# Optimization experiments

Measured on AMD Instinct MI355X. Metric: run time of the kernel, lower is better.

Reference implementation:

```python
import jax, jax.numpy as jnp
import numpy as np

B, N, D = 4, 2048, 1024
H = 16
HD = D // H


def setup_inputs() -> dict:
    key = jax.random.key(0)
    ks = jax.random.split(key, 6)
    x = jax.random.normal(ks[0], (B, N, D), dtype=jnp.float32)
    # additive causal mask: 0 on/below diagonal, -inf above
    neg = jnp.float32(-1e9)
    causal_mask = jnp.where(jnp.triu(jnp.ones((N, N), dtype=bool), k=1), neg, 0.0).astype(jnp.float32)
    s = 1.0 / np.sqrt(D)
    Wqkv = jax.random.normal(ks[1], (D, 3 * D), dtype=jnp.float32) * s
    bqkv = jax.random.normal(ks[2], (3 * D,), dtype=jnp.float32) * 0.01
    Wproj = jax.random.normal(ks[3], (D, D), dtype=jnp.float32) * s
    bproj = jax.random.normal(ks[4], (D,), dtype=jnp.float32) * 0.01
    return {"x": x, "causal_mask": causal_mask, "Wqkv": Wqkv, "bqkv": bqkv, "Wproj": Wproj, "bproj": bproj}


def reference(x, causal_mask, Wqkv, bqkv, Wproj, bproj):
    b, n, d = x.shape
    qkv = x @ Wqkv + bqkv  # [B,N,3D]
    qkv = qkv.reshape(b, n, 3, H, HD).transpose(2, 0, 3, 1, 4)  # [3,B,H,N,HD]
    q, k, v = qkv[0], qkv[1], qkv[2]
    scale = HD ** -0.5
    attn = jnp.einsum('bhqd,bhkd->bhqk', q, k) * scale  # [B,H,N,N]
    attn = attn + causal_mask  # broadcast [N,N] -> [B,H,N,N]
    attn = jax.nn.softmax(attn, axis=-1)
    out = jnp.einsum('bhqk,bhkd->bhqd', attn, v)  # [B,H,N,HD]
    out = out.transpose(0, 2, 1, 3).reshape(b, n, d)
    return out @ Wproj + bproj
```

## Files before the change

kernel.cpp:

```cpp
#include <hip/hip_runtime.h>
#include <hip/hip_bf16.h>

typedef unsigned short u16;
typedef unsigned int u32;
typedef __attribute__((ext_vector_type(8))) short bf16x8;
typedef __attribute__((ext_vector_type(4))) float f32x4;
typedef __attribute__((ext_vector_type(16))) float f32x16;

#define AS1(p) ((const __attribute__((address_space(1))) void*)(p))
#define AS3(p) ((__attribute__((address_space(3))) void*)(p))
#define STG(src, dst) __builtin_amdgcn_global_load_lds(AS1(src), AS3(dst), 16, 0, 0)

#if __has_builtin(__builtin_amdgcn_exp2f)
#define EXP2F(x) __builtin_amdgcn_exp2f(x)
#else
#define EXP2F(x) exp2f(x)
#endif

static __device__ __forceinline__ float b2f(u16 u) {
  union { unsigned int i; float f; } v; v.i = ((unsigned int)u) << 16; return v.f;
}
static __device__ __forceinline__ u16 f2b(float f) {
  union { float f; unsigned int i; } v; v.f = f;
  unsigned int r = v.i + 0x7FFFu + ((v.i >> 16) & 1u);
  return (u16)(r >> 16);
}
static __device__ __forceinline__ u32 cvt_pk_bf16(float lo, float hi) {
  u32 r;
  asm("v_cvt_pk_bf16_f32 %0, %1, %2" : "=v"(r) : "v"(lo), "v"(hi));
  return r;
}
static __device__ __forceinline__ void permswap(u32& a, u32& b) {
  asm("v_permlane32_swap_b32 %0, %1" : "+v"(a), "+v"(b));
}

__global__ __launch_bounds__(256) void cast_f32_bf16(const float* __restrict__ src,
                                                     u16* __restrict__ dst, int n8) {
  int stride = gridDim.x * blockDim.x;
  for (int i = blockIdx.x * blockDim.x + threadIdx.x; i < n8; i += stride) {
    const float4* s = (const float4*)(src + (size_t)i * 8);
    float4 a = s[0], b = s[1];
    bf16x8 o;
    o[0] = (short)f2b(a.x); o[1] = (short)f2b(a.y); o[2] = (short)f2b(a.z); o[3] = (short)f2b(a.w);
    o[4] = (short)f2b(b.x); o[5] = (short)f2b(b.y); o[6] = (short)f2b(b.z); o[7] = (short)f2b(b.w);
    *(bf16x8*)(dst + (size_t)i * 8) = o;
  }
}

__global__ __launch_bounds__(256) void transpose_w(const float* __restrict__ src,
                                                   u16* __restrict__ dst,
                                                   int R, int C) {
  __shared__ float tile[32][33];
  int c0 = blockIdx.x * 32, r0 = blockIdx.y * 32;
  int tx = threadIdx.x, ty = threadIdx.y;
  for (int i = ty; i < 32; i += 8) tile[i][tx] = src[(size_t)(r0 + i) * C + c0 + tx];
  __syncthreads();
  for (int i = ty; i < 32; i += 8) dst[(size_t)(c0 + i) * R + r0 + tx] = f2b(tile[tx][i]);
}

__global__ __launch_bounds__(256) void transpose_v(const u16* __restrict__ qkv,
                                                   u16* __restrict__ VT) {
  const int N = 2048, TD = 3072, D = 1024;
  int bh = blockIdx.y, n0 = blockIdx.x * 64;
  int b = bh >> 4, h = bh & 15;
  int tid = threadIdx.x;
  __shared__ u16 tl[64][72];
  #pragma unroll
  for (int i = 0; i < 16; ++i) {
    int idx = tid + i * 256;
    int nl = idx >> 6, dd = idx & 63;
    tl[dd][nl] = qkv[(size_t)(b * N + n0 + nl) * TD + 2 * D + h * 64 + dd];
  }
  __syncthreads();
  #pragma unroll
  for (int i = 0; i < 16; ++i) {
    int idx = tid + i * 256;
    int dd = idx >> 6, nl = idx & 63;
    VT[((size_t)bh * 64 + dd) * N + n0 + nl] = tl[dd][nl];
  }
}

template <typename OutT>
__global__ __launch_bounds__(256) void gemm_bt_bias(
    const u16* __restrict__ A,
    const u16* __restrict__ BT,
    const float* __restrict__ bias,
    OutT* __restrict__ C,
    int M, int N, int K) {
  __shared__ alignas(16) u16 Als[128 * 32];
  __shared__ alignas(16) u16 Bls[128 * 32];
  const int m0 = blockIdx.x * 128, n0 = blockIdx.y * 128;
  const int t = threadIdx.x;
  const int w = t >> 6, lane = t & 63;
  const int wr = w >> 1, wc = w & 1;
  const int rlo = lane & 15, g = lane >> 4;

  f32x4 acc[4][4] = {};

  const int r0 = t >> 2;
  const int c0 = (t & 3) << 3;
  const u16* aSrc = A + (size_t)(m0 + r0) * K + c0;
  const u16* bSrc = BT + (size_t)(n0 + r0) * K + c0;

  for (int k0 = 0; k0 < K; k0 += 32) {
    __builtin_amdgcn_global_load_lds(AS1(aSrc + k0), AS3(&Als[t * 8]), 16, 0, 0);
    __builtin_amdgcn_global_load_lds(AS1(aSrc + (size_t)64 * K + k0), AS3(&Als[(t + 256) * 8]), 16, 0, 0);
    __builtin_amdgcn_global_load_lds(AS1(bSrc + k0), AS3(&Bls[t * 8]), 16, 0, 0);
    __builtin_amdgcn_global_load_lds(AS1(bSrc + (size_t)64 * K + k0), AS3(&Bls[(t + 256) * 8]), 16, 0, 0);
    __syncthreads();

    bf16x8 a[4], b[4];
    #pragma unroll
    for (int m = 0; m < 4; ++m)
      a[m] = *(const bf16x8*)&Als[(wr * 64 + m * 16 + rlo) * 32 + g * 8];
    #pragma unroll
    for (int n = 0; n < 4; ++n)
      b[n] = *(const bf16x8*)&Bls[(wc * 64 + n * 16 + rlo) * 32 + g * 8];
    #pragma unroll
    for (int m = 0; m < 4; ++m)
      #pragma unroll
      for (int n = 0; n < 4; ++n)
        acc[m][n] = __builtin_amdgcn_mfma_f32_16x16x32_bf16(a[m], b[n], acc[m][n], 0, 0, 0);
    __syncthreads();
  }

  #pragma unroll
  for (int n = 0; n < 4; ++n) {
    const int col = n0 + wc * 64 + n * 16 + rlo;
    const float bv = bias[col];
    #pragma unroll
    for (int m = 0; m < 4; ++m) {
      const int row = m0 + wr * 64 + m * 16 + g * 4;
      #pragma unroll
      for (int i = 0; i < 4; ++i) {
        float r = acc[m][n][i] + bv;
        if constexpr (sizeof(OutT) == 2)
          C[(size_t)(row + i) * N + col] = (OutT)f2b(r);
        else
          C[(size_t)(row + i) * N + col] = (OutT)r;
      }
    }
  }
}

__global__ __launch_bounds__(256, 2) void attn_fwd(
    const u16* __restrict__ qkv,
    const u16* __restrict__ VT,
    u16* __restrict__ O) {
  const int N = 2048, TD = 3072, D = 1024;
  const int bid = blockIdx.x;
  const int qp = bid >> 6, bh = bid & 63;
  const int b = bh >> 4, h = bh & 15;
  const int t = threadIdx.x, w = t >> 6, lane = t & 63;
  const int l31 = lane & 31, hi = lane >> 5;
  const int qh = w >> 1, st = w & 1;

  __shared__ alignas(16) u16 pool16[2][2][64 * 64];
  __shared__ float rsLds[2][32];
  float* poolf = (float*)&pool16[0][0][0];

  const int c1 = t, c2 = t + 256;
  const int r1 = c1 >> 3, sc1 = ((c1 & 7) ^ (r1 & 7)) * 8;
  const int r2 = c2 >> 3, sc2 = ((c2 & 7) ^ (r2 & 7)) * 8;
  const u16* kbase = qkv + (size_t)(b * N) * TD + D + h * 64;
  const u16* vbase = VT + (size_t)bh * 64 * N;

#define ASTAGE(buf, j0) do { \
    STG(kbase + (size_t)((j0) + r1) * TD + sc1, &pool16[buf][0][c1 * 8]); \
    STG(kbase + (size_t)((j0) + r2) * TD + sc2, &pool16[buf][0][c2 * 8]); \
    STG(vbase + (size_t)r1 * N + (j0) + sc1, &pool16[buf][1][c1 * 8]); \
    STG(vbase + (size_t)r2 * N + (j0) + sc2, &pool16[buf][1][c2 * 8]); } while (0)

  const float L2E = 1.44269504089f;
  const float NSH = -23.0830992f;

  for (int pass = 0; pass < 2; ++pass) {
    const int qt = pass ? (15 - qp) : qp;
    const int qbw = qt * 128 + qh * 64;

    bf16x8 qf[2][4];
    #pragma unroll
    for (int qs = 0; qs < 2; ++qs) {
      const u16* qp_ = qkv + ((size_t)(b * N) + qbw + qs * 32 + l31) * TD + h * 64 + hi * 8;
      #pragma unroll
      for (int c = 0; c < 4; ++c) {
        bf16x8 v = *(const bf16x8*)(qp_ + c * 16);
        #pragma unroll
        for (int j = 0; j < 8; ++j)
          v[j] = (short)f2b(b2f((u16)v[j]) * 0.125f);
        qf[qs][c] = v;
      }
    }

    f32x16 o_acc[2][2] = {};
    float psum[2] = {0.f, 0.f};
    const int jend = qt * 128 + 64;

    ASTAGE(0, 0);
    __syncthreads();

    int cur = 0;
    for (int j0 = 0; j0 <= jend; j0 += 64) {
      if (j0 + 64 <= jend) ASTAGE(cur ^ 1, j0 + 64);

      const int sb2 = j0 + st * 32;
      if (sb2 <= qbw + 63) {
        bf16x8 kf[4];
        {
          const int row = st * 32 + l31, sw = (row & 7) << 3;
          #pragma unroll
          for (int c = 0; c < 4; ++c)
            kf[c] = *(const bf16x8*)&pool16[cur][0][row * 64 + ((c * 16 + hi * 8) ^ sw)];
        }
        bf16x8 vf[2][2];
        #pragma unroll
        for (int dt = 0; dt < 2; ++dt) {
          const int row = dt * 32 + l31, sw = (row & 7) << 3;
          #pragma unroll
          for (int kc = 0; kc < 2; ++kc)
            vf[kc][dt] = *(const bf16x8*)&pool16[cur][1][row * 64 + ((st * 32 + kc * 16 + hi * 8) ^ sw)];
        }

        #pragma unroll
        for (int qs = 0; qs < 2; ++qs) {
          if (qs == 0 && sb2 > qbw + 31) continue;
          const int qr = qbw + qs * 32 + l31;
          f32x16 S = {};
          __builtin_amdgcn_s_setprio(1);
          #pragma unroll
          for (int c = 0; c < 4; ++c)
            S = __builtin_amdgcn_mfma_f32_32x32x16_bf16(kf[c], qf[qs][c], S, 0, 0, 0);
          __builtin_amdgcn_s_setprio(0);
          if (sb2 + 31 > qbw + qs * 32) {
            const int kvb = sb2 + 4 * hi;
            #pragma unroll
            for (int r = 0; r < 16; ++r)
              if (kvb + (r & 3) + 8 * (r >> 2) > qr) S[r] = -1e30f;
          }
          float p[16];
          #pragma unroll
          for (int r = 0; r < 16; ++r) p[r] = EXP2F(fmaf(S[r], L2E, NSH));
          float ps = 0.f;
          #pragma unroll
          for (int r = 0; r < 16; ++r) ps += p[r];
          psum[qs] += ps;
          u32 wq[8];
          #pragma unroll
          for (int i = 0; i < 8; ++i) wq[i] = cvt_pk_bf16(p[2 * i], p[2 * i + 1]);
          permswap(wq[0], wq[2]); permswap(wq[1], wq[3]);
          permswap(wq[4], wq[6]); permswap(wq[5], wq[7]);
          union { u32 u[4]; bf16x8 v; } pa0, pa1;
          pa0.u[0] = wq[0]; pa0.u[1] = wq[1]; pa0.u[2] = wq[2]; pa0.u[3] = wq[3];
          pa1.u[0] = wq[4]; pa1.u[1] = wq[5]; pa1.u[2] = wq[6]; pa1.u[3] = wq[7];
          __builtin_amdgcn_s_setprio(1);
          #pragma unroll
          for (int dt = 0; dt < 2; ++dt) {
            o_acc[qs][dt] = __builtin_amdgcn_mfma_f32_32x32x16_bf16(pa0.v, vf[0][dt], o_acc[qs][dt], 0, 0, 0);
            o_acc[qs][dt] = __builtin_amdgcn_mfma_f32_32x32x16_bf16(pa1.v, vf[1][dt], o_acc[qs][dt], 0, 0, 0);
          }
          __builtin_amdgcn_s_setprio(0);
        }
      }
      __syncthreads();
      cur ^= 1;
    }

    float rsown[2];
    #pragma unroll
    for (int qs = 0; qs < 2; ++qs)
      rsown[qs] = psum[qs] + __shfl_xor(psum[qs], 32, 64);

    #pragma unroll
    for (int qs = 0; qs < 2; ++qs) {
      if (st != qs) {
        #pragma unroll
        for (int dt = 0; dt < 2; ++dt)
          #pragma unroll
          for (int r = 0; r < 16; ++r)
            poolf[qh * 2048 + (dt * 16 + r) * 64 + lane] = o_acc[qs][dt][r];
        rsLds[qh][l31] = rsown[qs];
      }
      __syncthreads();
      if (st == qs) {
        const float inv = 1.0f / (rsown[qs] + rsLds[qh][l31]);
        #pragma unroll
        for (int r = 0; r < 16; ++r) {
          const int qrow = (r & 3) + 8 * (r >> 2) + 4 * hi;
          const float invq = __shfl(inv, qrow, 64);
          const int q = qbw + qs * 32 + qrow;
          #pragma unroll
          for (int dt = 0; dt < 2; ++dt) {
            const float val = o_acc[qs][dt][r] + poolf[qh * 2048 + (dt * 16 + r) * 64 + lane];
            O[((size_t)(b * N) + q) * D + h * 64 + dt * 32 + l31] = f2b(val * invq);
          }
        }
      }
      __syncthreads();
    }
  }
#undef ASTAGE
}

extern "C" void kernel_launch(void* const* d_in, const int* in_sizes, int n_in,
                              void* d_out, int out_size, void* d_ws, size_t ws_size,
                              hipStream_t stream) {
  const float* x     = (const float*)d_in[0];
  const float* Wqkv  = (const float*)d_in[2];
  const float* bqkv  = (const float*)d_in[3];
  const float* Wproj = (const float*)d_in[4];
  const float* bproj = (const float*)d_in[5];
  float* out = (float*)d_out;

  const int B = 4, N = 2048, D = 1024, H = 16;
  const int BN = B * N;
  const int TD = 3 * D;

  char* ws = (char*)d_ws;
  u16* qkv    = (u16*)(ws);
  u16* vt     = (u16*)(ws + 50331648);
  u16* aout   = (u16*)(ws + 67108864);
  u16* wqkvT  = (u16*)(ws + 83886080);
  u16* wprojT = (u16*)(ws + 90177536);
  u16* xb     = (u16*)(ws + 92274688);

  cast_f32_bf16<<<2048, 256, 0, stream>>>(x, xb, BN * D / 8);
  transpose_w<<<dim3(TD / 32, D / 32), dim3(32, 8), 0, stream>>>(Wqkv, wqkvT, D, TD);
  transpose_w<<<dim3(D / 32, D / 32), dim3(32, 8), 0, stream>>>(Wproj, wprojT, D, D);
  gemm_bt_bias<u16><<<dim3(BN / 128, TD / 128), 256, 0, stream>>>(xb, wqkvT, bqkv, qkv, BN, TD, D);
  transpose_v<<<dim3(N / 64, B * H), 256, 0, stream>>>(qkv, vt);
  attn_fwd<<<512, 256, 0, stream>>>(qkv, vt, aout);
  gemm_bt_bias<float><<<dim3(BN / 128, D / 128), 256, 0, stream>>>(aout, wprojT, bproj, out, BN, D, D);
}
```

Measured before the change: 185.9 us.

## Merge prep kernels and write transposed V from QKV GEMM epilogue

Folds the x cast and both weight transposes into one launch that picks its role from the block index. The separate V-transpose kernel is removed: the QKV GEMM epilogue now also writes V columns straight into the transposed VT layout, using 8-byte stores of four consecutive rows. This saves two launches and a full read and write pass over V. In exchange the GEMM epilogue takes on extra scattered stores.

After: 178.6 us. 3.9% less time.

```diff
diff --git a/kernel.cpp b/kernel.cpp
--- a/kernel.cpp
+++ b/kernel.cpp
@@ -34,59 +34,41 @@
   asm("v_permlane32_swap_b32 %0, %1" : "+v"(a), "+v"(b));
 }
 
-__global__ __launch_bounds__(256) void cast_f32_bf16(const float* __restrict__ src,
-                                                     u16* __restrict__ dst, int n8) {
-  int stride = gridDim.x * blockDim.x;
-  for (int i = blockIdx.x * blockDim.x + threadIdx.x; i < n8; i += stride) {
-    const float4* s = (const float4*)(src + (size_t)i * 8);
-    float4 a = s[0], b = s[1];
-    bf16x8 o;
-    o[0] = (short)f2b(a.x); o[1] = (short)f2b(a.y); o[2] = (short)f2b(a.z); o[3] = (short)f2b(a.w);
-    o[4] = (short)f2b(b.x); o[5] = (short)f2b(b.y); o[6] = (short)f2b(b.z); o[7] = (short)f2b(b.w);
-    *(bf16x8*)(dst + (size_t)i * 8) = o;
+__global__ __launch_bounds__(256) void prep(const float* __restrict__ x, u16* __restrict__ xb,
+                                            const float* __restrict__ Wqkv, u16* __restrict__ wqkvT,
+                                            const float* __restrict__ Wproj, u16* __restrict__ wprojT) {
+  __shared__ float tile[32][33];
+  const int bid = blockIdx.x, t = threadIdx.x;
+  if (bid < 2048) {
+    const int n8 = 8192 * 1024 / 8;
+    for (int i = bid * 256 + t; i < n8; i += 2048 * 256) {
+      const float4* s = (const float4*)(x + (size_t)i * 8);
+      float4 a = s[0], b = s[1];
+      bf16x8 o;
+      o[0] = (short)f2b(a.x); o[1] = (short)f2b(a.y); o[2] = (short)f2b(a.z); o[3] = (short)f2b(a.w);
+      o[4] = (short)f2b(b.x); o[5] = (short)f2b(b.y); o[6] = (short)f2b(b.z); o[7] = (short)f2b(b.w);
+      *(bf16x8*)(xb + (size_t)i * 8) = o;
+    }
+  } else {
+    const float* src; u16* dst; int R, C, cx, ry;
+    if (bid < 5120) { const int l = bid - 2048; src = Wqkv; dst = wqkvT; R = 1024; C = 3072; cx = l % 96; ry = l / 96; }
+    else            { const int l = bid - 5120; src = Wproj; dst = wprojT; R = 1024; C = 1024; cx = l & 31; ry = l >> 5; }
+    const int c0 = cx * 32, r0 = ry * 32;
+    const int tx = t & 31, ty = t >> 5;
+    for (int i = ty; i < 32; i += 8) tile[i][tx] = src[(size_t)(r0 + i) * C + c0 + tx];
+    __syncthreads();
+    for (int i = ty; i < 32; i += 8) dst[(size_t)(c0 + i) * R + r0 + tx] = f2b(tile[tx][i]);
   }
 }
 
-__global__ __launch_bounds__(256) void transpose_w(const float* __restrict__ src,
-                                                   u16* __restrict__ dst,
-                                                   int R, int C) {
-  __shared__ float tile[32][33];
-  int c0 = blockIdx.x * 32, r0 = blockIdx.y * 32;
-  int tx = threadIdx.x, ty = threadIdx.y;
-  for (int i = ty; i < 32; i += 8) tile[i][tx] = src[(size_t)(r0 + i) * C + c0 + tx];
-  __syncthreads();
-  for (int i = ty; i < 32; i += 8) dst[(size_t)(c0 + i) * R + r0 + tx] = f2b(tile[tx][i]);
-}
-
-__global__ __launch_bounds__(256) void transpose_v(const u16* __restrict__ qkv,
-                                                   u16* __restrict__ VT) {
-  const int N = 2048, TD = 3072, D = 1024;
-  int bh = blockIdx.y, n0 = blockIdx.x * 64;
-  int b = bh >> 4, h = bh & 15;
-  int tid = threadIdx.x;
-  __shared__ u16 tl[64][72];
-  #pragma unroll
-  for (int i = 0; i < 16; ++i) {
-    int idx = tid + i * 256;
-    int nl = idx >> 6, dd = idx & 63;
-    tl[dd][nl] = qkv[(size_t)(b * N + n0 + nl) * TD + 2 * D + h * 64 + dd];
-  }
-  __syncthreads();
-  #pragma unroll
-  for (int i = 0; i < 16; ++i) {
-    int idx = tid + i * 256;
-    int dd = idx >> 6, nl = idx & 63;
-    VT[((size_t)bh * 64 + dd) * N + n0 + nl] = tl[dd][nl];
-  }
-}
-
-template <typename OutT>
+template <typename OutT, bool WVT>
 __global__ __launch_bounds__(256) void gemm_bt_bias(
     const u16* __restrict__ A,
     const u16* __restrict__ BT,
     const float* __restrict__ bias,
     OutT* __restrict__ C,
-    int M, int N, int K) {
+    int M, int N, int K,
+    u16* __restrict__ vt) {
   __shared__ alignas(16) u16 Als[128 * 32];
   __shared__ alignas(16) u16 Bls[128 * 32];
   const int m0 = blockIdx.x * 128, n0 = blockIdx.y * 128;
@@ -131,13 +113,28 @@
     #pragma unroll
     for (int m = 0; m < 4; ++m) {
       const int row = m0 + wr * 64 + m * 16 + g * 4;
+      u16 tmp[4];
       #pragma unroll
       for (int i = 0; i < 4; ++i) {
         float r = acc[m][n][i] + bv;
-        if constexpr (sizeof(OutT) == 2)
-          C[(size_t)(row + i) * N + col] = (OutT)f2b(r);
-        else
+        if constexpr (sizeof(OutT) == 2) {
+          const u16 hv = f2b(r);
+          C[(size_t)(row + i) * N + col] = (OutT)hv;
+          if constexpr (WVT) tmp[i] = hv;
+        } else {
           C[(size_t)(row + i) * N + col] = (OutT)r;
+        }
+      }
+      if constexpr (WVT) {
+        if (col >= 2048) {
+          const int cv = col - 2048;
+          const int h = cv >> 6, dd = cv & 63;
+          const int b = row >> 11, nloc = row & 2047;
+          uint2 pv;
+          pv.x = (u32)tmp[0] | ((u32)tmp[1] << 16);
+          pv.y = (u32)tmp[2] | ((u32)tmp[3] << 16);
+          *(uint2*)&vt[(((size_t)(b * 16 + h)) * 64 + dd) * 2048 + nloc] = pv;
+        }
       }
     }
   }
@@ -323,11 +320,8 @@
   u16* wprojT = (u16*)(ws + 90177536);
   u16* xb     = (u16*)(ws + 92274688);
 
-  cast_f32_bf16<<<2048, 256, 0, stream>>>(x, xb, BN * D / 8);
-  transpose_w<<<dim3(TD / 32, D / 32), dim3(32, 8), 0, stream>>>(Wqkv, wqkvT, D, TD);
-  transpose_w<<<dim3(D / 32, D / 32), dim3(32, 8), 0, stream>>>(Wproj, wprojT, D, D);
-  gemm_bt_bias<u16><<<dim3(BN / 128, TD / 128), 256, 0, stream>>>(xb, wqkvT, bqkv, qkv, BN, TD, D);
-  transpose_v<<<dim3(N / 64, B * H), 256, 0, stream>>>(qkv, vt);
+  prep<<<6144, 256, 0, stream>>>(x, xb, Wqkv, wqkvT, Wproj, wprojT);
+  gemm_bt_bias<u16, true><<<dim3(BN / 128, TD / 128), 256, 0, stream>>>(xb, wqkvT, bqkv, qkv, BN, TD, D, vt);
   attn_fwd<<<512, 256, 0, stream>>>(qkv, vt, aout);
-  gemm_bt_bias<float><<<dim3(BN / 128, D / 128), 256, 0, stream>>>(aout, wprojT, bproj, out, BN, D, D);
-}
+  gemm_bt_bias<float, false><<<dim3(BN / 128, D / 128), 256, 0, stream>>>(aout, wprojT, bproj, out, BN, D, D, nullptr);
+}
```
